# Kernel optimization log

Measured on AMD Instinct MI355X. Metric: run time of the kernel, lower is better.

## Reference

```python
import jax, jax.numpy as jnp
import numpy as np


def setup_inputs() -> dict:
    key = jax.random.key(0)
    x = jax.random.normal(key, (8, 4096, 512), dtype=jnp.float32)
    kappa = jnp.float32(0.5)
    return {"x": x, "kappa": kappa}


def reference(x, kappa):
    # Faithful reduction of DecorrLoss.forward (batched=False path).
    # Original math per flattened sample n (N = B*L samples, feature dim d):
    #   D_n = diag(x_n^2); V_n = D_n - I; C_n = x_n x_n^T - D_n
    #   corr = mean_n mean_{ij} C_n^2
    #   whit = mean_n mean_{ij} V_n^2
    #   grad = mean_n [(1-kappa)*C_n + kappa*V_n]
    # Algebraic identities avoid the O(N*d^2) intermediate:
    #   mean_{ij} C_n^2 = ((sum_i x_i^2)^2 - sum_i x_i^4) / d^2   (off-diag outer products)
    #   mean_{ij} V_n^2 = sum_i (x_i^2 - 1)^2 / d^2               (V is diagonal)
    #   mean_n C_n = X^T X / N with diagonal zeroed
    #   mean_n V_n = diag(mean_n x^2 - 1)
    b, l, d = x.shape
    xf = x.reshape(b * l, d)          # (N, d)
    n = xf.shape[0]
    x2 = xf * xf                      # (N, d)

    s2 = jnp.sum(x2, axis=1)          # (N,) sum of squares per sample
    s4 = jnp.sum(x2 * x2, axis=1)     # (N,) sum of fourth powers per sample
    inv_d2 = 1.0 / (d * d)
    correlation_loss = jnp.mean(s2 * s2 - s4) * inv_d2
    whitening_loss = jnp.mean(jnp.sum((x2 - 1.0) ** 2, axis=1)) * inv_d2

    gram = (xf.T @ xf) / n            # (d, d) = mean_n x_n x_n^T
    m2 = jnp.diagonal(gram)           # mean_n x_i^2
    off_diag = gram - jnp.diag(m2)    # mean_n C_n
    grad = (1.0 - kappa) * off_diag + kappa * jnp.diag(m2 - 1.0)
    return grad, correlation_loss, whitening_loss
```

## Files before the change

kernel.cpp:

```cpp
#include <hip/hip_runtime.h>
#include <hip/hip_bf16.h>
#include <stdint.h>


#define D 512
#define NSAMP 32768
#define KPARTS 32
#define KC 1024
#define BK_FB 64
#define NCHUNK 16
#define PREP_BLOCKS 1024

typedef __bf16 bf16x8 __attribute__((ext_vector_type(8)));
typedef float floatx4 __attribute__((ext_vector_type(4)));
typedef unsigned short ushort8 __attribute__((ext_vector_type(8)));
typedef __attribute__((address_space(1))) const uint32_t gas_u32;
typedef __attribute__((address_space(3))) uint32_t las_u32;

__global__ __launch_bounds__(1024) void zero_kernel(float* out, int n) {
    int i = blockIdx.x * 1024 + threadIdx.x;
    if (i < n) out[i] = 0.0f;
}


__global__ __launch_bounds__(256) void prep_kernel(const float* __restrict__ x,
                                                   uint16_t* __restrict__ xt,
                                                   float2* __restrict__ lpart) {
    __shared__ char lds[512 * 64];
    __shared__ float sA[4], sB[4];
    const int t = threadIdx.x;
    const int l = t & 63;
    const int w = t >> 6;
    const int bb = blockIdx.x;
    const int kc = bb >> 1;
    const int h = bb & 1;
    char* xtb = (char*)xt;

    const float* base = x + ((size_t)(32 * bb + 8 * w)) * D;
    float4 va[16];
#pragma unroll
    for (int r = 0; r < 8; ++r) {
        va[2 * r]     = *(const float4*)(base + (size_t)r * D + 4 * l);
        va[2 * r + 1] = *(const float4*)(base + (size_t)r * D + 256 + 4 * l);
    }

    float p2[8], p4[8];
#pragma unroll
    for (int r = 0; r < 8; ++r) {
        float a2 = 0.f, a4 = 0.f, e;
#pragma unroll
        for (int c = 0; c < 8; ++c) {
            const float v = ((const float*)&va[2 * r])[c];
            e = v * v;
            a2 += e;
            a4 += e * e;
        }
        p2[r] = a2;
        p4[r] = a4;
    }
#pragma unroll
    for (int m = 1; m < 64; m <<= 1) {
#pragma unroll
        for (int r = 0; r < 8; ++r) {
            p2[r] += __shfl_xor(p2[r], m);
            p4[r] += __shfl_xor(p4[r], m);
        }
    }
    float accA = 0.f, accB = 0.f;
#pragma unroll
    for (int r = 0; r < 8; ++r) {
        accA += p2[r] * p2[r] - p4[r];
        accB += p4[r] - 2.0f * p2[r];
    }

    ushort8 pk[8];
#pragma unroll
    for (int c2 = 0; c2 < 8; ++c2)
#pragma unroll
        for (int r = 0; r < 8; ++r)
            pk[c2][r] = __bfloat16_as_ushort(
                __float2bfloat16(((const float*)&va[2 * r + (c2 >> 2)])[c2 & 3]));

    const int pos_w = (w ^ (l & 3)) * 16;
#pragma unroll
    for (int c2 = 0; c2 < 8; ++c2) {
        const int f = (c2 < 4) ? (4 * l + c2) : (256 + 4 * l + (c2 - 4));
        *(ushort8*)(lds + f * 64 + pos_w) = pk[c2];
    }

    if (l == 0) { sA[w] = accA; sB[w] = accB; }
    __syncthreads();
    if (t == 0) {
        lpart[bb] = make_float2(sA[0] + sA[1] + sA[2] + sA[3],
                                sB[0] + sB[1] + sB[2] + sB[3]);
    }

    const int g = l & 3;
    const int g2 = h * 4 + g;
#pragma unroll
    for (int i = 0; i < 8; ++i) {
        const int f = i * 64 + w * 16 + (l >> 2);
        const int pos_r = (g ^ (l >> 4)) * 16;
        const ushort8 v = *(const ushort8*)(lds + f * 64 + pos_r);
        const size_t addr = (size_t)f * 65536 + (size_t)kc * 128 +
                            (size_t)(((g2 ^ (f & 7)) * 16));
        *(ushort8*)(xtb + addr) = v;
    }
}

__global__ __launch_bounds__(256, 2) void gram_bf16_kernel(const uint16_t* __restrict__ xt,
                                                           float* __restrict__ dst) {
    __shared__ __bf16 As[2][128 * 64];
    __shared__ __bf16 Bs[2][128 * 64];

    const int kpart = blockIdx.x & (KPARTS - 1);
    const int tile = blockIdx.x >> 5;
    const int i0 = (tile & 3) * 128;
    const int j0 = (tile >> 2) * 128;

    const int t = threadIdx.x;
    const int l = t & 63;
    const int wv = t >> 6;
    const char* xb = (const char*)xt;

    const int frow = wv * 32 + (l >> 3);
    const size_t ga = (size_t)(i0 + frow) * 65536 + (size_t)((l & 7) * 16);
    const size_t gb = (size_t)(j0 + frow) * 65536 + (size_t)((l & 7) * 16);

    floatx4 acc[4][4];
#pragma unroll
    for (int a = 0; a < 4; ++a)
#pragma unroll
        for (int b2 = 0; b2 < 4; ++b2) acc[a][b2] = (floatx4)0.0f;

    const int wm = (wv >> 1) * 64;
    const int wn = (wv & 1) * 64;
    const int rl = l & 15;
    const int q = l >> 4;

#define STAGE(c, buf)                                                                         \
    {                                                                                         \
        const size_t koff = (size_t)(kpart * 16 + (c)) * 128;                                 \
        _Pragma("unroll") for (int i = 0; i < 4; ++i) {                                       \
            __builtin_amdgcn_global_load_lds((gas_u32*)(xb + ga + (size_t)i * 8 * 65536 + koff), \
                                             (las_u32*)&As[buf][(wv * 32 + i * 8) * 64], 16, 0, 0); \
            __builtin_amdgcn_global_load_lds((gas_u32*)(xb + gb + (size_t)i * 8 * 65536 + koff), \
                                             (las_u32*)&Bs[buf][(wv * 32 + i * 8) * 64], 16, 0, 0); \
        }                                                                                     \
    }

    STAGE(0, 0);
    for (int c = 0; c < NCHUNK; ++c) {
        __syncthreads();
        if (c + 1 < NCHUNK) STAGE(c + 1, (c + 1) & 1);
        const char* Ab = (const char*)As[c & 1];
        const char* Bb = (const char*)Bs[c & 1];
#pragma unroll
        for (int kk = 0; kk < 2; ++kk) {
            const int qp = kk * 4 + q;
            bf16x8 af[4], bfr[4];
#pragma unroll
            for (int tm = 0; tm < 4; ++tm) {
                const int fi = wm + tm * 16 + rl;
                af[tm] = *(const bf16x8*)(Ab + fi * 128 + ((qp ^ (fi & 7)) * 16));
            }
#pragma unroll
            for (int tn = 0; tn < 4; ++tn) {
                const int fj = wn + tn * 16 + rl;
                bfr[tn] = *(const bf16x8*)(Bb + fj * 128 + ((qp ^ (fj & 7)) * 16));
            }
#pragma unroll
            for (int tm = 0; tm < 4; ++tm)
#pragma unroll
                for (int tn = 0; tn < 4; ++tn)
                    acc[tm][tn] = __builtin_amdgcn_mfma_f32_16x16x32_bf16(
                        af[tm], bfr[tn], acc[tm][tn], 0, 0, 0);
        }
    }
#undef STAGE

    float* p = dst + (size_t)kpart * (D * D);
#pragma unroll
    for (int tm = 0; tm < 4; ++tm)
#pragma unroll
        for (int tn = 0; tn < 4; ++tn)
#pragma unroll
            for (int rr = 0; rr < 4; ++rr) {
                const int gi = i0 + wm + tm * 16 + q * 4 + rr;
                const int gj = j0 + wn + tn * 16 + rl;
                p[(size_t)gi * D + gj] = acc[tm][tn][rr];
            }
}

__global__ __launch_bounds__(256) void finalize_fused_kernel(const float* __restrict__ src,
                                                             const float2* __restrict__ lpart,
                                                             const float* __restrict__ kappa_p,
                                                             float* __restrict__ out) {
    if (blockIdx.x == 256) {
        __shared__ float sA[4], sB[4];
        const int w = threadIdx.x >> 6;
        const int l = threadIdx.x & 63;
        float a = 0.f, b = 0.f;
        for (int i = threadIdx.x; i < PREP_BLOCKS; i += 256) {
            const float2 pp = lpart[i];
            a += pp.x;
            b += pp.y;
        }
#pragma unroll
        for (int m = 1; m < 64; m <<= 1) {
            a += __shfl_xor(a, m);
            b += __shfl_xor(b, m);
        }
        if (l == 0) { sA[w] = a; sB[w] = b; }
        __syncthreads();
        if (threadIdx.x == 0) {
            const float SCALE = 1.1641532182693481e-10f;
            out[D * D] = (sA[0] + sA[1] + sA[2] + sA[3]) * SCALE;
            out[D * D + 1] = (sB[0] + sB[1] + sB[2] + sB[3]) * SCALE + 0.001953125f;
        }
        return;
    }
    const int idx4 = blockIdx.x * 256 + threadIdx.x;
    const int base = idx4 * 4;
    float4 s = {0.f, 0.f, 0.f, 0.f};
    for (int p = 0; p < KPARTS; ++p) {
        const float4 v = *(const float4*)(src + (size_t)p * (D * D) + base);
        s.x += v.x; s.y += v.y; s.z += v.z; s.w += v.w;
    }
    const float kappa = *kappa_p;
    const float invn = 1.0f / (float)NSAMP;
    const int i = base >> 9;
    const int j = base & (D - 1);
    float r[4] = {s.x, s.y, s.z, s.w};
#pragma unroll
    for (int cpt = 0; cpt < 4; ++cpt) {
        const float m = r[cpt] * invn;
        r[cpt] = (i == j + cpt) ? kappa * (m - 1.0f) : (1.0f - kappa) * m;
    }
    float4 o = {r[0], r[1], r[2], r[3]};
    *(float4*)(out + base) = o;
}


__global__ __launch_bounds__(256) void loss_atomic_kernel(const float* __restrict__ x,
                                                          float* __restrict__ out) {
    __shared__ float sA[4], sB[4];
    const int w = threadIdx.x >> 6;
    const int l = threadIdx.x & 63;
    const int gw = blockIdx.x * 4 + w;
    const float* base = x + (size_t)gw * 4 * D;
    float4 v[8];
#pragma unroll
    for (int r = 0; r < 4; ++r) {
        v[2 * r]     = *(const float4*)(base + (size_t)r * D + l * 4);
        v[2 * r + 1] = *(const float4*)(base + (size_t)r * D + 256 + l * 4);
    }
    float p2[4], p4[4];
#pragma unroll
    for (int r = 0; r < 4; ++r) {
        const float* f = (const float*)&v[2 * r];
        float a2 = 0.f, a4 = 0.f, e;
#pragma unroll
        for (int c = 0; c < 8; ++c) { e = f[c] * f[c]; a2 += e; a4 += e * e; }
        p2[r] = a2; p4[r] = a4;
    }
#pragma unroll
    for (int m = 1; m < 64; m <<= 1) {
#pragma unroll
        for (int r = 0; r < 4; ++r) {
            p2[r] += __shfl_xor(p2[r], m);
            p4[r] += __shfl_xor(p4[r], m);
        }
    }
    float accA = 0.f, accB = 0.f;
#pragma unroll
    for (int r = 0; r < 4; ++r) {
        accA += p2[r] * p2[r] - p4[r];
        accB += p4[r] - 2.0f * p2[r];
    }
    if (l == 0) { sA[w] = accA; sB[w] = accB; }
    __syncthreads();
    if (threadIdx.x == 0) {
        const float SCALE = 1.1641532182693481e-10f;
        atomicAdd(out + D * D, (sA[0] + sA[1] + sA[2] + sA[3]) * SCALE);
        atomicAdd(out + D * D + 1, (sB[0] + sB[1] + sB[2] + sB[3]) * SCALE);
        if (blockIdx.x == 0) atomicAdd(out + D * D + 1, 0.001953125f);
    }
}

__global__ __launch_bounds__(256, 2) void gram_fp32_atomic_kernel(const float* __restrict__ x,
                                                                  float* __restrict__ dst) {
    __shared__ __bf16 As[128 * 64];
    __shared__ __bf16 Bs[128 * 64];
    char* Asb = (char*)As;
    char* Bsb = (char*)Bs;
    const int kpart = blockIdx.x & (KPARTS - 1);
    const int tile = blockIdx.x >> 5;
    const int i0 = (tile & 3) * 128;
    const int j0 = (tile >> 2) * 128;
    const int kbase = kpart * KC;
    const int t = threadIdx.x;
    const int l = t & 63;
    const int wv = t >> 6;
    const int fq = (l & 7) + 8 * wv;
    const int ksl = l >> 3;
    const float4* x4 = (const float4*)x;
    const int aoff = (i0 >> 2) + fq;
    const int boff = (j0 >> 2) + fq;
    float4 va[8], vb[8];
#pragma unroll
    for (int r = 0; r < 4; ++r) {
        const size_t row = (size_t)(kbase + 2 * ksl + 16 * r) * 128;
        va[2 * r] = x4[row + aoff];     va[2 * r + 1] = x4[row + 128 + aoff];
        vb[2 * r] = x4[row + boff];     vb[2 * r + 1] = x4[row + 128 + boff];
    }
    floatx4 acc[4][4];
#pragma unroll
    for (int a = 0; a < 4; ++a)
#pragma unroll
        for (int b = 0; b < 4; ++b) acc[a][b] = (floatx4)0.0f;
    const int wm = (wv >> 1) * 64;
    const int wn = (wv & 1) * 64;
    const int rl = l & 15;
    const int q = l >> 4;
    for (int c = 0; c < NCHUNK; ++c) {
        __syncthreads();
#pragma unroll
        for (int r = 0; r < 4; ++r) {
            const int k0 = 2 * ksl + 16 * r;
            const int g = k0 >> 3;
            const int sb = (k0 & 7) * 2;
            const float* fa0 = (const float*)&va[2 * r];
            const float* fa1 = (const float*)&va[2 * r + 1];
            const float* fb0 = (const float*)&vb[2 * r];
            const float* fb1 = (const float*)&vb[2 * r + 1];
#pragma unroll
            for (int cc = 0; cc < 4; ++cc) {
                const int f = fq * 4 + cc;
                const int off = f * 128 + ((g ^ (f & 7)) * 16) + sb;
                unsigned int pa = (unsigned int)__bfloat16_as_ushort(__float2bfloat16(fa0[cc])) |
                                  ((unsigned int)__bfloat16_as_ushort(__float2bfloat16(fa1[cc])) << 16);
                unsigned int pb = (unsigned int)__bfloat16_as_ushort(__float2bfloat16(fb0[cc])) |
                                  ((unsigned int)__bfloat16_as_ushort(__float2bfloat16(fb1[cc])) << 16);
                *(unsigned int*)(Asb + off) = pa;
                *(unsigned int*)(Bsb + off) = pb;
            }
        }
        if (c + 1 < NCHUNK) {
            const int kb = kbase + (c + 1) * BK_FB;
#pragma unroll
            for (int r = 0; r < 4; ++r) {
                const size_t row = (size_t)(kb + 2 * ksl + 16 * r) * 128;
                va[2 * r] = x4[row + aoff];     va[2 * r + 1] = x4[row + 128 + aoff];
                vb[2 * r] = x4[row + boff];     vb[2 * r + 1] = x4[row + 128 + boff];
            }
        }
        __syncthreads();
#pragma unroll
        for (int kk = 0; kk < 2; ++kk) {
            const int qp = kk * 4 + q;
            bf16x8 af[4], bfr[4];
#pragma unroll
            for (int tm = 0; tm < 4; ++tm) {
                const int fi = wm + tm * 16 + rl;
                af[tm] = *(const bf16x8*)(Asb + fi * 128 + ((qp ^ (fi & 7)) * 16));
            }
#pragma unroll
            for (int tn = 0; tn < 4; ++tn) {
                const int fj = wn + tn * 16 + rl;
                bfr[tn] = *(const bf16x8*)(Bsb + fj * 128 + ((qp ^ (fj & 7)) * 16));
            }
#pragma unroll
            for (int tm = 0; tm < 4; ++tm)
#pragma unroll
                for (int tn = 0; tn < 4; ++tn)
                    acc[tm][tn] = __builtin_amdgcn_mfma_f32_16x16x32_bf16(
                        af[tm], bfr[tn], acc[tm][tn], 0, 0, 0);
        }
    }
#pragma unroll
    for (int tm = 0; tm < 4; ++tm)
#pragma unroll
        for (int tn = 0; tn < 4; ++tn)
#pragma unroll
            for (int rr = 0; rr < 4; ++rr) {
                const int gi = i0 + wm + tm * 16 + q * 4 + rr;
                const int gj = j0 + wn + tn * 16 + rl;
                atomicAdd(dst + (size_t)gi * D + gj, acc[tm][tn][rr]);
            }
}

__global__ __launch_bounds__(256) void finalize1_kernel(const float* __restrict__ src,
                                                        const float* __restrict__ kappa_p,
                                                        float* __restrict__ out) {
    const int base = (blockIdx.x * 256 + threadIdx.x) * 4;
    float4 s = *(const float4*)(src + base);
    const float kappa = *kappa_p;
    const float invn = 1.0f / (float)NSAMP;
    const int i = base >> 9;
    const int j = base & (D - 1);
    float r[4] = {s.x, s.y, s.z, s.w};
#pragma unroll
    for (int cpt = 0; cpt < 4; ++cpt) {
        const float m = r[cpt] * invn;
        r[cpt] = (i == j + cpt) ? kappa * (m - 1.0f) : (1.0f - kappa) * m;
    }
    float4 o = {r[0], r[1], r[2], r[3]};
    *(float4*)(out + base) = o;
}

extern "C" void kernel_launch(void* const* d_in, const int* in_sizes, int n_in,
                              void* d_out, int out_size, void* d_ws, size_t ws_size,
                              hipStream_t stream) {
    const float* x = (const float*)d_in[0];
    const float* kappa = (const float*)d_in[1];
    float* out = (float*)d_out;

    const size_t xt_bytes = (size_t)D * NSAMP * sizeof(uint16_t);
    const size_t parts_bytes = (size_t)KPARTS * D * D * sizeof(float);
    const size_t lpart_bytes = (size_t)PREP_BLOCKS * sizeof(float2);

    if (ws_size >= xt_bytes + parts_bytes + lpart_bytes) {
        uint16_t* xt = (uint16_t*)d_ws;
        float* parts = (float*)((char*)d_ws + xt_bytes);
        float2* lpart = (float2*)((char*)d_ws + xt_bytes + parts_bytes);
        prep_kernel<<<PREP_BLOCKS, 256, 0, stream>>>(x, xt, lpart);
        gram_bf16_kernel<<<16 * KPARTS, 256, 0, stream>>>(xt, parts);
        finalize_fused_kernel<<<257, 256, 0, stream>>>(parts, lpart, kappa, out);
    } else {
        zero_kernel<<<(out_size + 1023) / 1024, 1024, 0, stream>>>(out, out_size);
        loss_atomic_kernel<<<2048, 256, 0, stream>>>(x, out);
        gram_fp32_atomic_kernel<<<16 * KPARTS, 256, 0, stream>>>(x, out);
        finalize1_kernel<<<(D * D / 4) / 256, 256, 0, stream>>>(out, kappa, out);
    }
}
```

Measured before the change: 128.9 us.

## Exploit Gram symmetry: compute upper-triangle tiles only, store bf16 partials

The Gram kernel now computes only the 10 upper-triangular 128x128 tiles instead of all 16. Diagonal tiles load a single operand and reuse it for both MFMA inputs. Work is split across 64 k-partitions with an XCD-aware block mapping, and the partials are stored as bf16 rather than fp32 to cut workspace traffic. The finalize kernel reduces these partials and writes both the tile and its transpose. This removes redundant MFMA work and partial-sum bandwidth, at the cost of extra rounding on the partials and strided transposed stores.

```diff
diff --git a/kernel.cpp b/kernel.cpp
--- a/kernel.cpp
+++ b/kernel.cpp
@@ -5,11 +5,14 @@
 
 #define D 512
 #define NSAMP 32768
-#define KPARTS 32
-#define KC 1024
+#define KPARTS 64
+#define NTILES 10
+#define NCHUNK 8
+#define PREP_BLOCKS 1024
+#define KPARTS_FB 32
+#define KC_FB 1024
 #define BK_FB 64
-#define NCHUNK 16
-#define PREP_BLOCKS 1024
+#define NCHUNK_FB 16
 
 typedef __bf16 bf16x8 __attribute__((ext_vector_type(8)));
 typedef float floatx4 __attribute__((ext_vector_type(4)));
@@ -108,15 +111,21 @@
     }
 }
 
-__global__ __launch_bounds__(256, 2) void gram_bf16_kernel(const uint16_t* __restrict__ xt,
-                                                           float* __restrict__ dst) {
+__global__ __launch_bounds__(256, 2) void gram_tri_kernel(const uint16_t* __restrict__ xt,
+                                                          uint16_t* __restrict__ parts) {
     __shared__ __bf16 As[2][128 * 64];
     __shared__ __bf16 Bs[2][128 * 64];
 
-    const int kpart = blockIdx.x & (KPARTS - 1);
-    const int tile = blockIdx.x >> 5;
-    const int i0 = (tile & 3) * 128;
-    const int j0 = (tile >> 2) * 128;
+    const int b = blockIdx.x;
+    const int xcd = b & 7;
+    const int s = b >> 3;
+    const int kpart = xcd + 8 * (s / NTILES);
+    const int tl = s % NTILES;
+    const int ti = (tl < 4) ? 0 : (tl < 7) ? 1 : (tl < 9) ? 2 : 3;
+    const int tj = (tl < 4) ? tl : (tl < 7) ? (tl - 3) : (tl < 9) ? (tl - 5) : 3;
+    const int i0 = ti * 128;
+    const int j0 = tj * 128;
+    const bool diag = (ti == tj);
 
     const int t = threadIdx.x;
     const int l = t & 63;
@@ -140,12 +149,16 @@
 
 #define STAGE(c, buf)                                                                         \
     {                                                                                         \
-        const size_t koff = (size_t)(kpart * 16 + (c)) * 128;                                 \
+        const size_t koff = (size_t)(kpart * NCHUNK + (c)) * 128;                             \
         _Pragma("unroll") for (int i = 0; i < 4; ++i) {                                       \
             __builtin_amdgcn_global_load_lds((gas_u32*)(xb + ga + (size_t)i * 8 * 65536 + koff), \
                                              (las_u32*)&As[buf][(wv * 32 + i * 8) * 64], 16, 0, 0); \
-            __builtin_amdgcn_global_load_lds((gas_u32*)(xb + gb + (size_t)i * 8 * 65536 + koff), \
-                                             (las_u32*)&Bs[buf][(wv * 32 + i * 8) * 64], 16, 0, 0); \
+        }                                                                                     \
+        if (!diag) {                                                                          \
+            _Pragma("unroll") for (int i = 0; i < 4; ++i) {                                   \
+                __builtin_amdgcn_global_load_lds((gas_u32*)(xb + gb + (size_t)i * 8 * 65536 + koff), \
+                                                 (las_u32*)&Bs[buf][(wv * 32 + i * 8) * 64], 16, 0, 0); \
+            }                                                                                 \
         }                                                                                     \
     }
 
@@ -154,7 +167,7 @@
         __syncthreads();
         if (c + 1 < NCHUNK) STAGE(c + 1, (c + 1) & 1);
         const char* Ab = (const char*)As[c & 1];
-        const char* Bb = (const char*)Bs[c & 1];
+        const char* Bb = diag ? Ab : (const char*)Bs[c & 1];
 #pragma unroll
         for (int kk = 0; kk < 2; ++kk) {
             const int qp = kk * 4 + q;
@@ -179,24 +192,24 @@
     }
 #undef STAGE
 
-    float* p = dst + (size_t)kpart * (D * D);
+    uint16_t* p = parts + ((size_t)kpart * NTILES + tl) * 16384;
 #pragma unroll
     for (int tm = 0; tm < 4; ++tm)
 #pragma unroll
         for (int tn = 0; tn < 4; ++tn)
 #pragma unroll
             for (int rr = 0; rr < 4; ++rr) {
-                const int gi = i0 + wm + tm * 16 + q * 4 + rr;
-                const int gj = j0 + wn + tn * 16 + rl;
-                p[(size_t)gi * D + gj] = acc[tm][tn][rr];
-            }
-}
-
-__global__ __launch_bounds__(256) void finalize_fused_kernel(const float* __restrict__ src,
-                                                             const float2* __restrict__ lpart,
-                                                             const float* __restrict__ kappa_p,
-                                                             float* __restrict__ out) {
-    if (blockIdx.x == 256) {
+                const int gi = wm + tm * 16 + q * 4 + rr;
+                const int gj = wn + tn * 16 + rl;
+                p[gi * 128 + gj] = __bfloat16_as_ushort(__float2bfloat16(acc[tm][tn][rr]));
+            }
+}
+
+__global__ __launch_bounds__(256) void finalize_tri_kernel(const uint16_t* __restrict__ parts,
+                                                           const float2* __restrict__ lpart,
+                                                           const float* __restrict__ kappa_p,
+                                                           float* __restrict__ out) {
+    if (blockIdx.x == 160) {
         __shared__ float sA[4], sB[4];
         const int w = threadIdx.x >> 6;
         const int l = threadIdx.x & 63;
@@ -220,25 +233,40 @@
         }
         return;
     }
-    const int idx4 = blockIdx.x * 256 + threadIdx.x;
-    const int base = idx4 * 4;
-    float4 s = {0.f, 0.f, 0.f, 0.f};
-    for (int p = 0; p < KPARTS; ++p) {
-        const float4 v = *(const float4*)(src + (size_t)p * (D * D) + base);
-        s.x += v.x; s.y += v.y; s.z += v.z; s.w += v.w;
+    const int tl = blockIdx.x / 16;
+    const int strip = blockIdx.x % 16;
+    const int ti = (tl < 4) ? 0 : (tl < 7) ? 1 : (tl < 9) ? 2 : 3;
+    const int tj = (tl < 4) ? tl : (tl < 7) ? (tl - 3) : (tl < 9) ? (tl - 5) : 3;
+
+    const int tr = threadIdx.x >> 5;
+    const int col0 = (threadIdx.x & 31) * 4;
+    const int r = strip * 8 + tr;
+
+    float s0 = 0.f, s1 = 0.f, s2 = 0.f, s3 = 0.f;
+    const uint16_t* base = parts + (size_t)tl * 16384 + r * 128 + col0;
+    for (int kp = 0; kp < KPARTS; ++kp) {
+        const ushort4 v = *(const ushort4*)(base + (size_t)kp * (NTILES * 16384));
+        s0 += __uint_as_float((uint32_t)v.x << 16);
+        s1 += __uint_as_float((uint32_t)v.y << 16);
+        s2 += __uint_as_float((uint32_t)v.z << 16);
+        s3 += __uint_as_float((uint32_t)v.w << 16);
     }
     const float kappa = *kappa_p;
     const float invn = 1.0f / (float)NSAMP;
-    const int i = base >> 9;
-    const int j = base & (D - 1);
-    float r[4] = {s.x, s.y, s.z, s.w};
-#pragma unroll
-    for (int cpt = 0; cpt < 4; ++cpt) {
-        const float m = r[cpt] * invn;
-        r[cpt] = (i == j + cpt) ? kappa * (m - 1.0f) : (1.0f - kappa) * m;
-    }
-    float4 o = {r[0], r[1], r[2], r[3]};
-    *(float4*)(out + base) = o;
+    const int gi = ti * 128 + r;
+    const int gj0 = tj * 128 + col0;
+    float rr[4] = {s0, s1, s2, s3};
+#pragma unroll
+    for (int c = 0; c < 4; ++c) {
+        const float m = rr[c] * invn;
+        rr[c] = (gi == gj0 + c) ? kappa * (m - 1.0f) : (1.0f - kappa) * m;
+    }
+    float4 o = {rr[0], rr[1], rr[2], rr[3]};
+    *(float4*)(out + (size_t)gi * D + gj0) = o;
+    if (ti != tj) {
+#pragma unroll
+        for (int c = 0; c < 4; ++c) out[(size_t)(gj0 + c) * D + gi] = rr[c];
+    }
 }
 
 
@@ -294,11 +322,11 @@
     __shared__ __bf16 Bs[128 * 64];
     char* Asb = (char*)As;
     char* Bsb = (char*)Bs;
-    const int kpart = blockIdx.x & (KPARTS - 1);
+    const int kpart = blockIdx.x & (KPARTS_FB - 1);
     const int tile = blockIdx.x >> 5;
     const int i0 = (tile & 3) * 128;
     const int j0 = (tile >> 2) * 128;
-    const int kbase = kpart * KC;
+    const int kbase = kpart * KC_FB;
     const int t = threadIdx.x;
     const int l = t & 63;
     const int wv = t >> 6;
@@ -323,7 +351,7 @@
     const int wn = (wv & 1) * 64;
     const int rl = l & 15;
     const int q = l >> 4;
-    for (int c = 0; c < NCHUNK; ++c) {
+    for (int c = 0; c < NCHUNK_FB; ++c) {
         __syncthreads();
 #pragma unroll
         for (int r = 0; r < 4; ++r) {
@@ -346,7 +374,7 @@
                 *(unsigned int*)(Bsb + off) = pb;
             }
         }
-        if (c + 1 < NCHUNK) {
+        if (c + 1 < NCHUNK_FB) {
             const int kb = kbase + (c + 1) * BK_FB;
 #pragma unroll
             for (int r = 0; r < 4; ++r) {
@@ -417,20 +445,20 @@
     float* out = (float*)d_out;
 
     const size_t xt_bytes = (size_t)D * NSAMP * sizeof(uint16_t);
-    const size_t parts_bytes = (size_t)KPARTS * D * D * sizeof(float);
+    const size_t parts_bytes = (size_t)KPARTS * NTILES * 16384 * sizeof(uint16_t);
     const size_t lpart_bytes = (size_t)PREP_BLOCKS * sizeof(float2);
 
     if (ws_size >= xt_bytes + parts_bytes + lpart_bytes) {
         uint16_t* xt = (uint16_t*)d_ws;
-        float* parts = (float*)((char*)d_ws + xt_bytes);
+        uint16_t* parts = (uint16_t*)((char*)d_ws + xt_bytes);
         float2* lpart = (float2*)((char*)d_ws + xt_bytes + parts_bytes);
         prep_kernel<<<PREP_BLOCKS, 256, 0, stream>>>(x, xt, lpart);
-        gram_bf16_kernel<<<16 * KPARTS, 256, 0, stream>>>(xt, parts);
-        finalize_fused_kernel<<<257, 256, 0, stream>>>(parts, lpart, kappa, out);
+        gram_tri_kernel<<<8 * NTILES * (KPARTS / 8), 256, 0, stream>>>(xt, parts);
+        finalize_tri_kernel<<<161, 256, 0, stream>>>(parts, lpart, kappa, out);
     } else {
         zero_kernel<<<(out_size + 1023) / 1024, 1024, 0, stream>>>(out, out_size);
         loss_atomic_kernel<<<2048, 256, 0, stream>>>(x, out);
-        gram_fp32_atomic_kernel<<<16 * KPARTS, 256, 0, stream>>>(x, out);
+        gram_fp32_atomic_kernel<<<16 * KPARTS_FB, 256, 0, stream>>>(x, out);
         finalize1_kernel<<<(D * D / 4) / 256, 256, 0, stream>>>(out, kappa, out);
     }
 }
```

After: 123.2 us. 1.05x faster.
